# Kernel tuning notes

Hardware: AMD Instinct MI355X
Metric: run time of the kernel (lower is better)

Reference implementation:

```python
import jax, jax.numpy as jnp
import numpy as np

EMBED_DIM = 512
NUM_HEADS = 8
HEAD_DIM = EMBED_DIM // NUM_HEADS  # 64


def setup_inputs() -> dict:
    key = jax.random.key(0)
    ks = jax.random.split(key, 9)
    B, N, E, H, D = 4, 1024, EMBED_DIM, NUM_HEADS, HEAD_DIM
    s = 1.0 / np.sqrt(E)  # ~ nn.Linear init scale
    x = jax.random.normal(ks[0], (B, N, E), dtype=jnp.float32)
    # weights stored as (in, out): y = x @ W + b (same math as torch x @ W.T)
    Wq = jax.random.uniform(ks[1], (E, E), jnp.float32, -s, s)
    bq = jax.random.uniform(ks[2], (E,), jnp.float32, -s, s)
    Wk = jax.random.uniform(ks[3], (E, E), jnp.float32, -s, s)
    bk = jax.random.uniform(ks[4], (E,), jnp.float32, -s, s)
    Wv = jax.random.uniform(ks[5], (E, E), jnp.float32, -s, s)
    bv = jax.random.uniform(ks[6], (E,), jnp.float32, -s, s)
    Wg = jax.random.uniform(ks[7], (E, H * D * D), jnp.float32, -s, s)
    bg = jax.random.uniform(ks[8], (H * D * D,), jnp.float32, -s, s)
    return {"x": x, "Wq": Wq, "bq": bq, "Wk": Wk, "bk": bk,
            "Wv": Wv, "bv": bv, "Wg": Wg, "bg": bg}


def reference(x, Wq, bq, Wk, bk, Wv, bv, Wg, bg):
    B, N, E = x.shape
    H, D = NUM_HEADS, HEAD_DIM
    # per-token generated transform g: [B, N, H, D, D] (act = exact GELU)
    g = jax.nn.gelu(x @ Wg + bg, approximate=False).reshape(B, N, H, D, D)
    q = (x @ Wq + bq).reshape(B, N, H, D)
    k = (x @ Wk + bk).reshape(B, N, H, D)
    v = (x @ Wv + bv).reshape(B, N, H, D)
    # q' = q @ g  (per-token, per-head 1xD @ DxD)
    qg = jnp.einsum("bnhd,bnhde->bnhe", q, g)
    # attention scores (note: no 1/sqrt(d) scaling in the original)
    att = jnp.einsum("bnhe,bmhe->bhnm", qg, k)
    att = jax.nn.softmax(att, axis=-1)
    out = jnp.einsum("bhnm,bmhd->bnhd", att, v)
    return out.reshape(B, N, E)
```

## Files before the change

### kernel.cpp

```cpp
#include <hip/hip_runtime.h>
#include <math.h>

#define TOK   4096
#define EDIM  512
#define HEADS 8
#define DHEAD 64
#define GCOLS 32768

typedef unsigned short u16;
typedef _Float16 f16;
typedef __attribute__((ext_vector_type(8))) f16 f16x8;
typedef __attribute__((ext_vector_type(4))) f16 f16x4;
typedef __attribute__((ext_vector_type(4))) float f32x4;
typedef __attribute__((ext_vector_type(4))) unsigned short u16x4;

typedef const __attribute__((address_space(1))) void* gas_ptr;
typedef __attribute__((address_space(3))) void* las_ptr;

__device__ __forceinline__ void gll16(const void* g, void* lds) {
  __builtin_amdgcn_global_load_lds((gas_ptr)g, (las_ptr)lds, 16, 0, 0);
}

__device__ __forceinline__ u16 f2h_bits(float f) {
  union { f16 h; u16 u; } v; v.h = (f16)f;
  return v.u;
}

__device__ __forceinline__ float fast_gelu(float x) {
  float s = x * 0.7071067811865475f;
  float ax = fabsf(s);
  float t = 1.0f / (1.0f + 0.3275911f * ax);
  float poly = t * (0.254829592f + t * (-0.284496736f + t * (1.421413741f +
               t * (-1.453152027f + t * 1.061405429f))));
  float e = __expf(-ax * ax);
  float r = 1.0f - poly * e;
  float erfv = copysignf(r, s);
  return 0.5f * x * (1.0f + erfv);
}

__global__ void cast_f16_k(const float* __restrict__ in, u16* __restrict__ out, int n) {
  int i = (blockIdx.x * blockDim.x + threadIdx.x) * 4;
  if (i + 3 < n) {
    float4 f = *(const float4*)(in + i);
    u16x4 h;
    h.x = f2h_bits(f.x); h.y = f2h_bits(f.y);
    h.z = f2h_bits(f.z); h.w = f2h_bits(f.w);
    *(u16x4*)(out + i) = h;
  }
}

__global__ void transpose_f16_k(const float* __restrict__ in, u16* __restrict__ out,
                                int K, int N) {
  __shared__ float tile[32][33];
  int n0 = blockIdx.x * 32, k0 = blockIdx.y * 32;
  int tx = threadIdx.x, ty = threadIdx.y;
  #pragma unroll
  for (int i = 0; i < 4; i++)
    tile[ty + i * 8][tx] = in[(size_t)(k0 + ty + i * 8) * N + n0 + tx];
  __syncthreads();
  #pragma unroll
  for (int i = 0; i < 4; i++)
    out[(size_t)(n0 + ty + i * 8) * K + k0 + tx] = f2h_bits(tile[tx][ty + i * 8]);
}

__global__ __launch_bounds__(256, 2) void qkv_gemm_k(
    const u16* __restrict__ xf, const u16* __restrict__ Wqt,
    const u16* __restrict__ Wkt, const u16* __restrict__ Wvt,
    const float* __restrict__ bq, const float* __restrict__ bk, const float* __restrict__ bv,
    u16* __restrict__ qho, u16* __restrict__ ko, u16* __restrict__ vTo) {
  __shared__ __align__(16) u16 As[16 * 512];
  __shared__ __align__(16) u16 Bs[16 * 512];
  const int which = blockIdx.z;
  const u16* Wt = which == 0 ? Wqt : (which == 1 ? Wkt : Wvt);
  const float* bias = which == 0 ? bq : (which == 1 ? bk : bv);
  const int m0 = blockIdx.x * 128;
  const int n0 = blockIdx.y * 128;
  const int tid = threadIdx.x;
  const int w = tid >> 6, lane = tid & 63, l15 = lane & 15, quad = lane >> 4;
  const int mhalf = w >> 1, nhalf = w & 1;

  f32x4 acc[4][4];
  #pragma unroll
  for (int i = 0; i < 4; i++)
    #pragma unroll
    for (int j = 0; j < 4; j++) acc[i][j] = f32x4{0.f, 0.f, 0.f, 0.f};

  for (int kk = 0; kk < 512; kk += 64) {
    #pragma unroll
    for (int i = 0; i < 8; i++) {
      int cb = w * 8 + i;
      if (cb < 16) {
        int ks = cb >> 3, mt = cb & 7;
        gll16(xf + (size_t)(m0 + mt * 16 + l15) * 512 + kk + ks * 32 + quad * 8,
              As + cb * 512);
      } else {
        int bi = cb - 16, ks = bi >> 3, nt = bi & 7;
        gll16(Wt + (size_t)(n0 + nt * 16 + l15) * 512 + kk + ks * 32 + quad * 8,
              Bs + bi * 512);
      }
    }
    __syncthreads();
    #pragma unroll
    for (int ks = 0; ks < 2; ks++) {
      f16x8 a[4], b[4];
      #pragma unroll
      for (int mt = 0; mt < 4; mt++)
        a[mt] = *(const f16x8*)(As + (ks * 8 + mhalf * 4 + mt) * 512 + lane * 8);
      #pragma unroll
      for (int nt = 0; nt < 4; nt++)
        b[nt] = *(const f16x8*)(Bs + (ks * 8 + nhalf * 4 + nt) * 512 + lane * 8);
      #pragma unroll
      for (int mt = 0; mt < 4; mt++)
        #pragma unroll
        for (int nt = 0; nt < 4; nt++)
          acc[mt][nt] = __builtin_amdgcn_mfma_f32_16x16x32_f16(a[mt], b[nt], acc[mt][nt], 0, 0, 0);
    }
    __syncthreads();
  }
  #pragma unroll
  for (int nt = 0; nt < 4; nt++) {
    int col = n0 + (nhalf * 4 + nt) * 16 + l15;
    float bia = bias[col];
    int h = col >> 6, d = col & 63;
    #pragma unroll
    for (int mt = 0; mt < 4; mt++) {
      #pragma unroll
      for (int r = 0; r < 4; r++) {
        int t = m0 + (mhalf * 4 + mt) * 16 + quad * 4 + r;
        int b_ = t >> 10, n = t & 1023;
        float val = acc[mt][nt][r] + bia;
        size_t idx = (((size_t)(b_ * 8 + h) * 1024) + n) * 64 + d;
        if (which == 0)      qho[idx] = f2h_bits(val);
        else if (which == 1) ko[idx] = f2h_bits(val);
        else                 vTo[(((size_t)(b_ * 8 + h) * 64) + d) * 1024 + n] = f2h_bits(val);
      }
    }
  }
}

__global__ __launch_bounds__(512, 4) void qg_fused_k(
    const u16* __restrict__ xf, const u16* __restrict__ Wgt,
    const float* __restrict__ bg, const u16* __restrict__ qh,
    float* __restrict__ qgp) {
  __shared__ __align__(16) u16 As[16 * 512];
  __shared__ __align__(16) u16 Bs[32 * 512];
  __shared__ __align__(16) u16 Qs[128 * 64];
  const int head = blockIdx.x & 7;
  const int jh = (blockIdx.x >> 3) & 1;
  const int t0 = (blockIdx.x >> 4) * 128;
  const int tid = threadIdx.x;
  const int w = tid >> 6, lane = tid & 63, l15 = lane & 15, quad = lane >> 4;
  const int mhalf = w >> 2;
  const int ntA = w & 3;
  const int b_ = t0 >> 10, nseq0 = t0 & 1023;
  const u16* qbase = qh + (((size_t)(b_ * 8 + head) * 1024) + nseq0) * 64;

  #pragma unroll
  for (int i = 0; i < 2; i++) {
    int cb = w * 2 + i;
    gll16(qbase + (size_t)cb * 512 + (size_t)lane * 8, Qs + (size_t)cb * 512);
  }
  f32x4 qg[4];
  #pragma unroll
  for (int i = 0; i < 4; i++) qg[i] = f32x4{0.f, 0.f, 0.f, 0.f};
  __syncthreads();

  for (int jp = 0; jp < 8; jp++) {
    const int j0 = jh * 16 + jp * 2;
    const int c0 = head * 4096 + j0 * 128;
    f32x4 zacc[4][4];
    #pragma unroll
    for (int i = 0; i < 4; i++)
      #pragma unroll
      for (int z = 0; z < 4; z++) zacc[i][z] = f32x4{0.f, 0.f, 0.f, 0.f};

    for (int kk = 0; kk < 512; kk += 64) {
      #pragma unroll
      for (int i = 0; i < 6; i++) {
        int cb = w * 6 + i;
        if (cb < 16) {
          int ks = cb >> 3, mt = cb & 7;
          gll16(xf + (size_t)(t0 + mt * 16 + l15) * 512 + kk + ks * 32 + quad * 8,
                As + cb * 512);
        } else {
          int bi = cb - 16, ks = bi >> 4, nt = bi & 15;
          gll16(Wgt + (size_t)(c0 + nt * 16 + l15) * 512 + kk + ks * 32 + quad * 8,
                Bs + bi * 512);
        }
      }
      __syncthreads();
      #pragma unroll
      for (int ks = 0; ks < 2; ks++) {
        f16x8 a[4];
        #pragma unroll
        for (int mt = 0; mt < 4; mt++)
          a[mt] = *(const f16x8*)(As + (ks * 8 + mhalf * 4 + mt) * 512 + lane * 8);
        #pragma unroll
        for (int z = 0; z < 4; z++) {
          int nt = (z >> 1) * 8 + (z & 1) * 4 + ntA;
          f16x8 b = *(const f16x8*)(Bs + (ks * 16 + nt) * 512 + lane * 8);
          #pragma unroll
          for (int mt = 0; mt < 4; mt++)
            zacc[mt][z] = __builtin_amdgcn_mfma_f32_16x16x32_f16(a[mt], b, zacc[mt][z], 0, 0, 0);
        }
      }
      __syncthreads();
    }
    float bgv[4];
    #pragma unroll
    for (int z = 0; z < 4; z++) {
      int nt = (z >> 1) * 8 + (z & 1) * 4 + ntA;
      bgv[z] = bg[c0 + nt * 16 + l15];
    }
    const int d0 = 2 * j0;
    #pragma unroll
    for (int mt = 0; mt < 4; mt++) {
      #pragma unroll
      for (int r = 0; r < 4; r++) {
        int row = mhalf * 64 + mt * 16 + quad * 4 + r;
        f16x4 qp = *(const f16x4*)(Qs + row * 64 + d0);
        float g0 = fast_gelu(zacc[mt][0][r] + bgv[0]);
        float g1 = fast_gelu(zacc[mt][1][r] + bgv[1]);
        float g2 = fast_gelu(zacc[mt][2][r] + bgv[2]);
        float g3 = fast_gelu(zacc[mt][3][r] + bgv[3]);
        qg[mt][r] += (float)qp.x * g0 + (float)qp.y * g1 +
                     (float)qp.z * g2 + (float)qp.w * g3;
      }
    }
  }
  float* qout = qgp + (size_t)jh * TOK * EDIM;
  const int eb = ntA * 16;
  #pragma unroll
  for (int mt = 0; mt < 4; mt++) {
    #pragma unroll
    for (int r = 0; r < 4; r++) {
      int t = t0 + mhalf * 64 + mt * 16 + quad * 4 + r;
      int bb = t >> 10, n = t & 1023;
      qout[(((size_t)(bb * 8 + head) * 1024) + n) * 64 + eb + l15] = qg[mt][r];
    }
  }
}

__global__ __launch_bounds__(256, 2) void attn_k(
    const float* __restrict__ qgp, const u16* __restrict__ kb,
    const u16* __restrict__ vTb, float* __restrict__ out) {
  __shared__ __align__(16) u16 Ks[8 * 512];
  __shared__ __align__(16) u16 Vs[8 * 512];
  __shared__ __align__(16) f16 Ps[4][16 * 72];
  const int idx = blockIdx.x;
  const int bh = idx & 31;
  const int qt = idx >> 5;
  const int b_ = bh >> 3, h = bh & 7;
  const int tid = threadIdx.x;
  const int w = tid >> 6, lane = tid & 63, l15 = lane & 15, quad = lane >> 4;

  const float* qg0 = qgp + (size_t)bh * 1024 * 64;
  const float* qg1 = qg0 + (size_t)TOK * EDIM;
  const u16* kB  = kb  + (size_t)bh * 1024 * 64;
  const u16* vB  = vTb + (size_t)bh * 64 * 1024;

  f16x8 aq[2];
  #pragma unroll
  for (int ks = 0; ks < 2; ks++) {
    size_t off = (size_t)(qt * 64 + w * 16 + l15) * 64 + ks * 32 + quad * 8;
    f16x8 v;
    #pragma unroll
    for (int e = 0; e < 8; e++)
      v[e] = (f16)(qg0[off + e] + qg1[off + e]);
    aq[ks] = v;
  }

  f32x4 o[4];
  #pragma unroll
  for (int i = 0; i < 4; i++) o[i] = f32x4{0.f, 0.f, 0.f, 0.f};
  float m_old[4], l_old[4];
  #pragma unroll
  for (int r = 0; r < 4; r++) { m_old[r] = -1e30f; l_old[r] = 0.f; }

  for (int kt = 0; kt < 16; kt++) {
    #pragma unroll
    for (int i = 0; i < 2; i++) {
      int cb = w * 2 + i;
      int ks = cb >> 2, nt = cb & 3;
      gll16(kB + (size_t)(kt * 64 + nt * 16 + l15) * 64 + ks * 32 + quad * 8, Ks + cb * 512);
      gll16(vB + (size_t)(nt * 16 + l15) * 1024 + kt * 64 + ks * 32 + quad * 8, Vs + cb * 512);
    }
    __syncthreads();
    f32x4 s[4];
    #pragma unroll
    for (int nt = 0; nt < 4; nt++) s[nt] = f32x4{0.f, 0.f, 0.f, 0.f};
    #pragma unroll
    for (int ks = 0; ks < 2; ks++)
      #pragma unroll
      for (int nt = 0; nt < 4; nt++) {
        f16x8 kf = *(const f16x8*)(Ks + (ks * 4 + nt) * 512 + lane * 8);
        s[nt] = __builtin_amdgcn_mfma_f32_16x16x32_f16(aq[ks], kf, s[nt], 0, 0, 0);
      }
    float rmax[4];
    #pragma unroll
    for (int r = 0; r < 4; r++)
      rmax[r] = fmaxf(fmaxf(s[0][r], s[1][r]), fmaxf(s[2][r], s[3][r]));
    #pragma unroll
    for (int off = 1; off < 16; off <<= 1)
      #pragma unroll
      for (int r = 0; r < 4; r++)
        rmax[r] = fmaxf(rmax[r], __shfl_xor(rmax[r], off));
    float alpha[4], rsum[4];
    #pragma unroll
    for (int r = 0; r < 4; r++) {
      float mn = fmaxf(m_old[r], rmax[r]);
      alpha[r] = __expf(m_old[r] - mn);
      m_old[r] = mn;
      rsum[r] = 0.f;
    }
    #pragma unroll
    for (int nt = 0; nt < 4; nt++)
      #pragma unroll
      for (int r = 0; r < 4; r++) {
        float p = __expf(s[nt][r] - m_old[r]);
        rsum[r] += p;
        Ps[w][(quad * 4 + r) * 72 + nt * 16 + l15] = (f16)p;
      }
    #pragma unroll
    for (int off = 1; off < 16; off <<= 1)
      #pragma unroll
      for (int r = 0; r < 4; r++)
        rsum[r] += __shfl_xor(rsum[r], off);
    #pragma unroll
    for (int r = 0; r < 4; r++) l_old[r] = l_old[r] * alpha[r] + rsum[r];
    #pragma unroll
    for (int nt = 0; nt < 4; nt++)
      #pragma unroll
      for (int r = 0; r < 4; r++) o[nt][r] *= alpha[r];
    #pragma unroll
    for (int ks = 0; ks < 2; ks++) {
      f16x8 pa = *(const f16x8*)(&Ps[w][l15 * 72 + ks * 32 + quad * 8]);
      #pragma unroll
      for (int nt = 0; nt < 4; nt++) {
        f16x8 vf = *(const f16x8*)(Vs + (ks * 4 + nt) * 512 + lane * 8);
        o[nt] = __builtin_amdgcn_mfma_f32_16x16x32_f16(pa, vf, o[nt], 0, 0, 0);
      }
    }
    __syncthreads();
  }
  #pragma unroll
  for (int r = 0; r < 4; r++) {
    float inv = 1.f / l_old[r];
    int n = qt * 64 + w * 16 + quad * 4 + r;
    #pragma unroll
    for (int nt = 0; nt < 4; nt++)
      out[((size_t)(b_ * 1024 + n)) * 512 + h * 64 + nt * 16 + l15] = o[nt][r] * inv;
  }
}

extern "C" void kernel_launch(void* const* d_in, const int* in_sizes, int n_in,
                              void* d_out, int out_size, void* d_ws, size_t ws_size,
                              hipStream_t stream) {
  const float* x  = (const float*)d_in[0];
  const float* Wq = (const float*)d_in[1];
  const float* bq = (const float*)d_in[2];
  const float* Wk = (const float*)d_in[3];
  const float* bk = (const float*)d_in[4];
  const float* Wv = (const float*)d_in[5];
  const float* bv = (const float*)d_in[6];
  const float* Wg = (const float*)d_in[7];
  const float* bg = (const float*)d_in[8];
  float* out = (float*)d_out;

  const size_t NX = (size_t)TOK * EDIM;
  const size_t NWG = (size_t)GCOLS * EDIM;
  const size_t NW = (size_t)EDIM * EDIM;

  char* p = (char*)d_ws;
  u16* xf  = (u16*)p; p += NX * 2;
  u16* Wgt = (u16*)p; p += NWG * 2;
  u16* Wqt = (u16*)p; p += NW * 2;
  u16* Wkt = (u16*)p; p += NW * 2;
  u16* Wvt = (u16*)p; p += NW * 2;
  u16* qh  = (u16*)p; p += NX * 2;
  u16* kf  = (u16*)p; p += NX * 2;
  u16* vT  = (u16*)p; p += NX * 2;
  float* qgp = (float*)p; p += NX * 4 * 2;

  hipLaunchKernelGGL(cast_f16_k, dim3(NX / 1024), dim3(256), 0, stream,
                     x, xf, (int)NX);
  hipLaunchKernelGGL(transpose_f16_k, dim3(EDIM / 32, EDIM / 32), dim3(32, 8), 0, stream,
                     Wq, Wqt, EDIM, EDIM);
  hipLaunchKernelGGL(transpose_f16_k, dim3(EDIM / 32, EDIM / 32), dim3(32, 8), 0, stream,
                     Wk, Wkt, EDIM, EDIM);
  hipLaunchKernelGGL(transpose_f16_k, dim3(EDIM / 32, EDIM / 32), dim3(32, 8), 0, stream,
                     Wv, Wvt, EDIM, EDIM);
  hipLaunchKernelGGL(transpose_f16_k, dim3(GCOLS / 32, EDIM / 32), dim3(32, 8), 0, stream,
                     Wg, Wgt, EDIM, GCOLS);
  hipLaunchKernelGGL(qkv_gemm_k, dim3(TOK / 128, EDIM / 128, 3), dim3(256), 0, stream,
                     xf, Wqt, Wkt, Wvt, bq, bk, bv, qh, kf, vT);
  hipLaunchKernelGGL(qg_fused_k, dim3(512), dim3(512), 0, stream,
                     xf, Wgt, bg, qh, qgp);
  hipLaunchKernelGGL(attn_k, dim3(512), dim3(256), 0, stream,
                     qgp, kf, vT, out);
}
```

Before: 481.8 us.

## Double-buffer LDS staging in QKV and QG GEMMs, vectorize weight transpose

The QKV and fused QG GEMMs now use two LDS buffers, so global-to-LDS loads for the next k-step are issued before computing the current one. This removes one barrier per step, and in the QG kernel the nested jp/kk loops become a single 64-step stream with the GELU epilogue folded in. The weight transpose now uses 64x64 tiles with float4 reads and 16-byte half writes. Doubling LDS lowers the QG kernel's launch-bound occupancy target from 4 to 2 blocks, which may reduce latency hiding.

New measurement: 501.9 us. 4.2% more time.

```diff
diff --git a/kernel.cpp b/kernel.cpp
--- a/kernel.cpp
+++ b/kernel.cpp
@@ -13,6 +13,7 @@
 typedef __attribute__((ext_vector_type(4))) f16 f16x4;
 typedef __attribute__((ext_vector_type(4))) float f32x4;
 typedef __attribute__((ext_vector_type(4))) unsigned short u16x4;
+typedef __attribute__((ext_vector_type(8))) unsigned short u16x8;
 
 typedef const __attribute__((address_space(1))) void* gas_ptr;
 typedef __attribute__((address_space(3))) void* las_ptr;
@@ -51,16 +52,29 @@
 
 __global__ void transpose_f16_k(const float* __restrict__ in, u16* __restrict__ out,
                                 int K, int N) {
-  __shared__ float tile[32][33];
-  int n0 = blockIdx.x * 32, k0 = blockIdx.y * 32;
-  int tx = threadIdx.x, ty = threadIdx.y;
-  #pragma unroll
-  for (int i = 0; i < 4; i++)
-    tile[ty + i * 8][tx] = in[(size_t)(k0 + ty + i * 8) * N + n0 + tx];
+  __shared__ u16 tileT[64][72];
+  const int n0 = blockIdx.x * 64, k0 = blockIdx.y * 64;
+  const int tid = threadIdx.x;
+  const int kl = tid >> 4;
+  const int nl4 = (tid & 15) * 4;
+  #pragma unroll
+  for (int i = 0; i < 4; i++) {
+    int k = kl + i * 16;
+    float4 f = *(const float4*)(in + (size_t)(k0 + k) * N + n0 + nl4);
+    tileT[nl4 + 0][k] = f2h_bits(f.x);
+    tileT[nl4 + 1][k] = f2h_bits(f.y);
+    tileT[nl4 + 2][k] = f2h_bits(f.z);
+    tileT[nl4 + 3][k] = f2h_bits(f.w);
+  }
   __syncthreads();
-  #pragma unroll
-  for (int i = 0; i < 4; i++)
-    out[(size_t)(n0 + ty + i * 8) * K + k0 + tx] = f2h_bits(tile[tx][ty + i * 8]);
+  const int nr = tid >> 3;
+  const int ks = (tid & 7) * 8;
+  #pragma unroll
+  for (int p = 0; p < 2; p++) {
+    int n = nr + p * 32;
+    u16x8 v = *(const u16x8*)&tileT[n][ks];
+    *(u16x8*)(out + (size_t)(n0 + n) * K + k0 + ks) = v;
+  }
 }
 
 __global__ __launch_bounds__(256, 2) void qkv_gemm_k(
@@ -68,8 +82,8 @@
     const u16* __restrict__ Wkt, const u16* __restrict__ Wvt,
     const float* __restrict__ bq, const float* __restrict__ bk, const float* __restrict__ bv,
     u16* __restrict__ qho, u16* __restrict__ ko, u16* __restrict__ vTo) {
-  __shared__ __align__(16) u16 As[16 * 512];
-  __shared__ __align__(16) u16 Bs[16 * 512];
+  __shared__ __align__(16) u16 As[2][16 * 512];
+  __shared__ __align__(16) u16 Bs[2][16 * 512];
   const int which = blockIdx.z;
   const u16* Wt = which == 0 ? Wqt : (which == 1 ? Wkt : Wvt);
   const float* bias = which == 0 ? bq : (which == 1 ? bk : bv);
@@ -79,36 +93,43 @@
   const int w = tid >> 6, lane = tid & 63, l15 = lane & 15, quad = lane >> 4;
   const int mhalf = w >> 1, nhalf = w & 1;
 
-  f32x4 acc[4][4];
-  #pragma unroll
-  for (int i = 0; i < 4; i++)
-    #pragma unroll
-    for (int j = 0; j < 4; j++) acc[i][j] = f32x4{0.f, 0.f, 0.f, 0.f};
-
-  for (int kk = 0; kk < 512; kk += 64) {
+  auto stage = [&](int s) {
+    int kk = s * 64, buf = s & 1;
     #pragma unroll
     for (int i = 0; i < 8; i++) {
       int cb = w * 8 + i;
       if (cb < 16) {
         int ks = cb >> 3, mt = cb & 7;
         gll16(xf + (size_t)(m0 + mt * 16 + l15) * 512 + kk + ks * 32 + quad * 8,
-              As + cb * 512);
+              &As[buf][cb * 512]);
       } else {
         int bi = cb - 16, ks = bi >> 3, nt = bi & 7;
         gll16(Wt + (size_t)(n0 + nt * 16 + l15) * 512 + kk + ks * 32 + quad * 8,
-              Bs + bi * 512);
-      }
-    }
-    __syncthreads();
+              &Bs[buf][bi * 512]);
+      }
+    }
+  };
+
+  f32x4 acc[4][4];
+  #pragma unroll
+  for (int i = 0; i < 4; i++)
+    #pragma unroll
+    for (int j = 0; j < 4; j++) acc[i][j] = f32x4{0.f, 0.f, 0.f, 0.f};
+
+  stage(0);
+  __syncthreads();
+  for (int s = 0; s < 8; s++) {
+    if (s < 7) stage(s + 1);
+    int buf = s & 1;
     #pragma unroll
     for (int ks = 0; ks < 2; ks++) {
       f16x8 a[4], b[4];
       #pragma unroll
       for (int mt = 0; mt < 4; mt++)
-        a[mt] = *(const f16x8*)(As + (ks * 8 + mhalf * 4 + mt) * 512 + lane * 8);
+        a[mt] = *(const f16x8*)(&As[buf][(ks * 8 + mhalf * 4 + mt) * 512 + lane * 8]);
       #pragma unroll
       for (int nt = 0; nt < 4; nt++)
-        b[nt] = *(const f16x8*)(Bs + (ks * 8 + nhalf * 4 + nt) * 512 + lane * 8);
+        b[nt] = *(const f16x8*)(&Bs[buf][(ks * 8 + nhalf * 4 + nt) * 512 + lane * 8]);
       #pragma unroll
       for (int mt = 0; mt < 4; mt++)
         #pragma unroll
@@ -138,12 +159,12 @@
   }
 }
 
-__global__ __launch_bounds__(512, 4) void qg_fused_k(
+__global__ __launch_bounds__(512, 2) void qg_fused_k(
     const u16* __restrict__ xf, const u16* __restrict__ Wgt,
     const float* __restrict__ bg, const u16* __restrict__ qh,
     float* __restrict__ qgp) {
-  __shared__ __align__(16) u16 As[16 * 512];
-  __shared__ __align__(16) u16 Bs[32 * 512];
+  __shared__ __align__(16) u16 As[2][16 * 512];
+  __shared__ __align__(16) u16 Bs[2][32 * 512];
   __shared__ __align__(16) u16 Qs[128 * 64];
   const int head = blockIdx.x & 7;
   const int jh = (blockIdx.x >> 3) & 1;
@@ -155,78 +176,89 @@
   const int b_ = t0 >> 10, nseq0 = t0 & 1023;
   const u16* qbase = qh + (((size_t)(b_ * 8 + head) * 1024) + nseq0) * 64;
 
+  auto stage = [&](int s) {
+    int jp = s >> 3, kk = (s & 7) * 64, buf = s & 1;
+    int c0s = head * 4096 + (jh * 16 + jp * 2) * 128;
+    #pragma unroll
+    for (int i = 0; i < 6; i++) {
+      int cb = w * 6 + i;
+      if (cb < 16) {
+        int ks = cb >> 3, mt = cb & 7;
+        gll16(xf + (size_t)(t0 + mt * 16 + l15) * 512 + kk + ks * 32 + quad * 8,
+              &As[buf][cb * 512]);
+      } else {
+        int bi = cb - 16, ks = bi >> 4, nt = bi & 15;
+        gll16(Wgt + (size_t)(c0s + nt * 16 + l15) * 512 + kk + ks * 32 + quad * 8,
+              &Bs[buf][bi * 512]);
+      }
+    }
+  };
+
   #pragma unroll
   for (int i = 0; i < 2; i++) {
     int cb = w * 2 + i;
     gll16(qbase + (size_t)cb * 512 + (size_t)lane * 8, Qs + (size_t)cb * 512);
   }
+  stage(0);
+
   f32x4 qg[4];
   #pragma unroll
   for (int i = 0; i < 4; i++) qg[i] = f32x4{0.f, 0.f, 0.f, 0.f};
+  f32x4 zacc[4][4];
+  #pragma unroll
+  for (int i = 0; i < 4; i++)
+    #pragma unroll
+    for (int z = 0; z < 4; z++) zacc[i][z] = f32x4{0.f, 0.f, 0.f, 0.f};
+
   __syncthreads();
 
-  for (int jp = 0; jp < 8; jp++) {
-    const int j0 = jh * 16 + jp * 2;
-    const int c0 = head * 4096 + j0 * 128;
-    f32x4 zacc[4][4];
-    #pragma unroll
-    for (int i = 0; i < 4; i++)
-      #pragma unroll
-      for (int z = 0; z < 4; z++) zacc[i][z] = f32x4{0.f, 0.f, 0.f, 0.f};
-
-    for (int kk = 0; kk < 512; kk += 64) {
-      #pragma unroll
-      for (int i = 0; i < 6; i++) {
-        int cb = w * 6 + i;
-        if (cb < 16) {
-          int ks = cb >> 3, mt = cb & 7;
-          gll16(xf + (size_t)(t0 + mt * 16 + l15) * 512 + kk + ks * 32 + quad * 8,
-                As + cb * 512);
-        } else {
-          int bi = cb - 16, ks = bi >> 4, nt = bi & 15;
-          gll16(Wgt + (size_t)(c0 + nt * 16 + l15) * 512 + kk + ks * 32 + quad * 8,
-                Bs + bi * 512);
-        }
-      }
-      __syncthreads();
-      #pragma unroll
-      for (int ks = 0; ks < 2; ks++) {
-        f16x8 a[4];
+  for (int s = 0; s < 64; s++) {
+    if (s < 63) stage(s + 1);
+    const int buf = s & 1;
+    #pragma unroll
+    for (int ks = 0; ks < 2; ks++) {
+      f16x8 a[4];
+      #pragma unroll
+      for (int mt = 0; mt < 4; mt++)
+        a[mt] = *(const f16x8*)(&As[buf][(ks * 8 + mhalf * 4 + mt) * 512 + lane * 8]);
+      #pragma unroll
+      for (int z = 0; z < 4; z++) {
+        int nt = (z >> 1) * 8 + (z & 1) * 4 + ntA;
+        f16x8 b = *(const f16x8*)(&Bs[buf][(ks * 16 + nt) * 512 + lane * 8]);
         #pragma unroll
         for (int mt = 0; mt < 4; mt++)
-          a[mt] = *(const f16x8*)(As + (ks * 8 + mhalf * 4 + mt) * 512 + lane * 8);
+          zacc[mt][z] = __builtin_amdgcn_mfma_f32_16x16x32_f16(a[mt], b, zacc[mt][z], 0, 0, 0);
+      }
+    }
+    if ((s & 7) == 7) {
+      const int jp = s >> 3;
+      const int j0 = jh * 16 + jp * 2;
+      const int c0 = head * 4096 + j0 * 128;
+      float bgv[4];
+      #pragma unroll
+      for (int z = 0; z < 4; z++) {
+        int nt = (z >> 1) * 8 + (z & 1) * 4 + ntA;
+        bgv[z] = bg[c0 + nt * 16 + l15];
+      }
+      const int d0 = 2 * j0;
+      #pragma unroll
+      for (int mt = 0; mt < 4; mt++) {
         #pragma unroll
-        for (int z = 0; z < 4; z++) {
-          int nt = (z >> 1) * 8 + (z & 1) * 4 + ntA;
-          f16x8 b = *(const f16x8*)(Bs + (ks * 16 + nt) * 512 + lane * 8);
-          #pragma unroll
-          for (int mt = 0; mt < 4; mt++)
-            zacc[mt][z] = __builtin_amdgcn_mfma_f32_16x16x32_f16(a[mt], b, zacc[mt][z], 0, 0, 0);
+        for (int r = 0; r < 4; r++) {
+          int row = mhalf * 64 + mt * 16 + quad * 4 + r;
+          f16x4 qp = *(const f16x4*)(Qs + row * 64 + d0);
+          float g0 = fast_gelu(zacc[mt][0][r] + bgv[0]);
+          float g1 = fast_gelu(zacc[mt][1][r] + bgv[1]);
+          float g2 = fast_gelu(zacc[mt][2][r] + bgv[2]);
+          float g3 = fast_gelu(zacc[mt][3][r] + bgv[3]);
+          qg[mt][r] += (float)qp.x * g0 + (float)qp.y * g1 +
+                       (float)qp.z * g2 + (float)qp.w * g3;
+          zacc[mt][0][r] = 0.f; zacc[mt][1][r] = 0.f;
+          zacc[mt][2][r] = 0.f; zacc[mt][3][r] = 0.f;
         }
       }
-      __syncthreads();
-    }
-    float bgv[4];
-    #pragma unroll
-    for (int z = 0; z < 4; z++) {
-      int nt = (z >> 1) * 8 + (z & 1) * 4 + ntA;
-      bgv[z] = bg[c0 + nt * 16 + l15];
-    }
-    const int d0 = 2 * j0;
-    #pragma unroll
-    for (int mt = 0; mt < 4; mt++) {
-      #pragma unroll
-      for (int r = 0; r < 4; r++) {
-        int row = mhalf * 64 + mt * 16 + quad * 4 + r;
-        f16x4 qp = *(const f16x4*)(Qs + row * 64 + d0);
-        float g0 = fast_gelu(zacc[mt][0][r] + bgv[0]);
-        float g1 = fast_gelu(zacc[mt][1][r] + bgv[1]);
-        float g2 = fast_gelu(zacc[mt][2][r] + bgv[2]);
-        float g3 = fast_gelu(zacc[mt][3][r] + bgv[3]);
-        qg[mt][r] += (float)qp.x * g0 + (float)qp.y * g1 +
-                     (float)qp.z * g2 + (float)qp.w * g3;
-      }
-    }
+    }
+    __syncthreads();
   }
   float* qout = qgp + (size_t)jh * TOK * EDIM;
   const int eb = ntA * 16;
@@ -384,13 +416,13 @@
 
   hipLaunchKernelGGL(cast_f16_k, dim3(NX / 1024), dim3(256), 0, stream,
                      x, xf, (int)NX);
-  hipLaunchKernelGGL(transpose_f16_k, dim3(EDIM / 32, EDIM / 32), dim3(32, 8), 0, stream,
+  hipLaunchKernelGGL(transpose_f16_k, dim3(EDIM / 64, EDIM / 64), dim3(256), 0, stream,
                      Wq, Wqt, EDIM, EDIM);
-  hipLaunchKernelGGL(transpose_f16_k, dim3(EDIM / 32, EDIM / 32), dim3(32, 8), 0, stream,
+  hipLaunchKernelGGL(transpose_f16_k, dim3(EDIM / 64, EDIM / 64), dim3(256), 0, stream,
                      Wk, Wkt, EDIM, EDIM);
-  hipLaunchKernelGGL(transpose_f16_k, dim3(EDIM / 32, EDIM / 32), dim3(32, 8), 0, stream,
+  hipLaunchKernelGGL(transpose_f16_k, dim3(EDIM / 64, EDIM / 64), dim3(256), 0, stream,
                      Wv, Wvt, EDIM, EDIM);
-  hipLaunchKernelGGL(transpose_f16_k, dim3(GCOLS / 32, EDIM / 32), dim3(32, 8), 0, stream,
+  hipLaunchKernelGGL(transpose_f16_k, dim3(GCOLS / 64, EDIM / 64), dim3(256), 0, stream,
                      Wg, Wgt, EDIM, GCOLS);
   hipLaunchKernelGGL(qkv_gemm_k, dim3(TOK / 128, EDIM / 128, 3), dim3(256), 0, stream,
                      xf, Wqt, Wkt, Wvt, bq, bk, bv, qh, kf, vT);
```
